# Kernel tuning notes

Hardware: AMD Instinct MI355X
Metric: run time of the kernel (lower is better)

## Reference

```python
import jax, jax.numpy as jnp
import numpy as np

B, N, C, H = 16, 4096, 256, 4
D = C // H


def setup_inputs() -> dict:
    key = jax.random.key(0)
    ks = jax.random.split(key, 16)
    s = 0.02
    inp = {
        "x": jax.random.normal(ks[0], (B, N, C), jnp.float32),
        "encoding": jax.random.normal(ks[1], (2, B, 1, N, D), jnp.float32),
        "Wqkv_w": jax.random.normal(ks[2], (3 * C, C), jnp.float32) * s,
        "Wqkv_b": jnp.zeros((3 * C,), jnp.float32),
        "tssa_qkv_w": jax.random.normal(ks[3], (C, C), jnp.float32) * s,
        "tssa_qkv_b": jnp.zeros((C,), jnp.float32),
        "temp": jnp.ones((H, 1), jnp.float32),
        "tssa_out_w": jax.random.normal(ks[4], (C, C), jnp.float32) * s,
        "tssa_out_b": jnp.zeros((C,), jnp.float32),
        "out_proj_w": jax.random.normal(ks[5], (C, C), jnp.float32) * s,
        "out_proj_b": jnp.zeros((C,), jnp.float32),
        "ffn1_w": jax.random.normal(ks[6], (2 * C, 2 * C), jnp.float32) * s,
        "ffn1_b": jnp.zeros((2 * C,), jnp.float32),
        "ln_g": jnp.ones((2 * C,), jnp.float32),
        "ln_b": jnp.zeros((2 * C,), jnp.float32),
        "ffn2_w": jax.random.normal(ks[7], (C, 2 * C), jnp.float32) * s,
        "ffn2_b": jnp.zeros((C,), jnp.float32),
    }
    return inp


def _rotate_half(t):
    # (..., d) -> pairwise rotate: (x1, x2) -> (-x2, x1)
    t2 = t.reshape(t.shape[:-1] + (-1, 2))
    x1, x2 = t2[..., 0], t2[..., 1]
    return jnp.stack((-x2, x1), axis=-1).reshape(t.shape)


def reference(x, encoding, Wqkv_w, Wqkv_b, tssa_qkv_w, tssa_qkv_b, temp,
              tssa_out_w, tssa_out_b, out_proj_w, out_proj_b,
              ffn1_w, ffn1_b, ln_g, ln_b, ffn2_w, ffn2_b):
    b, n, c = x.shape
    h, d = H, D
    # QKV projection, layout (h, d, 3) on last dim as in unflatten(-1,(h,-1,3))
    qkv = (x @ Wqkv_w.T + Wqkv_b).reshape(b, n, h, d, 3).transpose(0, 2, 1, 3, 4)  # b h n d 3
    q, k, v = qkv[..., 0], qkv[..., 1], qkv[..., 2]
    rope = lambda t: t * encoding[0] + _rotate_half(t) * encoding[1]
    q = rope(q)
    k = rope(k)
    flat = lambda t: t.transpose(0, 2, 1, 3).reshape(b, n, c)  # b h n d -> b n (h d)
    w_input = (flat(q) + flat(k) + flat(v)) / 3.0
    # TSSA attention
    w = (w_input @ tssa_qkv_w.T + tssa_qkv_b).reshape(b, n, h, d).transpose(0, 2, 1, 3)  # b h n d
    norm = jnp.sqrt(jnp.sum(w * w, axis=2, keepdims=True))  # L2 over sequence axis N
    w_normed = w / jnp.maximum(norm, 1e-12)
    sum_ws = jnp.sum(w_normed * w_normed, axis=-1)  # b h n
    Pi = jax.nn.softmax(sum_ws * temp[None, :, :], axis=1)  # softmax over heads
    Pi_norm = Pi / (jnp.sum(Pi, axis=-1, keepdims=True) + 1e-8)
    dots = jnp.einsum('bhn,bhnd->bh', Pi_norm, w * w)  # (b,h,1,d) summed over d
    attn = 1.0 / (1.0 + dots)  # b h
    out = -(w * Pi[..., None]) * attn[:, :, None, None]  # b h n d
    out = out.transpose(0, 2, 1, 3).reshape(b, n, c)
    context = out @ tssa_out_w.T + tssa_out_b
    message = context @ out_proj_w.T + out_proj_b
    # residual FFN
    cat = jnp.concatenate([x, message], axis=-1)  # b n 2c
    h1 = cat @ ffn1_w.T + ffn1_b
    mu = jnp.mean(h1, axis=-1, keepdims=True)
    var = jnp.mean((h1 - mu) ** 2, axis=-1, keepdims=True)
    ln = (h1 - mu) / jnp.sqrt(var + 1e-5) * ln_g + ln_b
    g = jax.nn.gelu(ln, approximate=False)
    return x + (g @ ffn2_w.T + ffn2_b)
```

## Files before the change

### kernel.cpp

```cpp
#include <hip/hip_runtime.h>
#include <math.h>

#define Bc 16
#define Nc 4096

typedef __attribute__((ext_vector_type(8))) short short8;
typedef __attribute__((ext_vector_type(4))) float floatx4;

__device__ __forceinline__ unsigned short f2bf(float f) {
    union { float f; unsigned int u; } v; v.f = f;
    unsigned int u = v.u;
    return (unsigned short)((u + 0x7fffu + ((u >> 16) & 1u)) >> 16);
}
__device__ __forceinline__ float bf2f(unsigned short u) {
    union { unsigned int u; float f; } v; v.u = ((unsigned int)u) << 16;
    return v.f;
}

__device__ __forceinline__ void gll16(const unsigned short* g, unsigned short* l) {
    __builtin_amdgcn_global_load_lds(
        (const __attribute__((address_space(1))) void*)g,
        (__attribute__((address_space(3))) void*)l,
        16, 0, 0);
}

template <int EPI, typename TOUT>
__global__ __launch_bounds__(512) void gemm_bf(
    const unsigned short* __restrict__ A0, int lda0,
    const unsigned short* __restrict__ A1, int lda1, int K0,
    const unsigned short* __restrict__ W,
    const float* __restrict__ bias,
    const unsigned short* __restrict__ resid_bf,
    const float* __restrict__ Pi,
    const float* __restrict__ attnb,
    float* __restrict__ norm2,
    float* __restrict__ rowstats,
    TOUT* __restrict__ C, int N, int K)
{
    __shared__ alignas(16) unsigned short As[128 * 64];
    __shared__ alignas(16) unsigned short Bs[256 * 64];

    const int t = threadIdx.x;
    const int bn = blockIdx.x, bm = blockIdx.y;
    const int lane = t & 63, wave = t >> 6;
    const int wm = wave >> 2, wn = wave & 3;
    const int quad = lane >> 4, l16 = lane & 15;
    const int rt = t >> 3, st = t & 7;

    floatx4 acc[4][4];
    #pragma unroll
    for (int i = 0; i < 4; ++i)
        #pragma unroll
        for (int j = 0; j < 4; ++j)
            acc[i][j] = (floatx4){0.f, 0.f, 0.f, 0.f};

    for (int k0 = 0; k0 < K; k0 += 64) {
        #pragma unroll
        for (int hh = 0; hh < 2; ++hh) {
            const int row = hh * 64 + rt;
            const int col = k0 + (st ^ (row & 7)) * 8;
            unsigned short* ldsa = As + row * 64 + st * 8;
            const size_t grow = (size_t)bm * 128 + row;
            if constexpr (EPI == 2) {
                const int b = (int)(grow >> 12);
                const int hd = col >> 6;
                const float sc = -Pi[grow * 4 + hd] * attnb[b * 4 + hd];
                const short8 a = *(const short8*)(A0 + grow * (size_t)lda0 + col);
                short8 o;
                #pragma unroll
                for (int j = 0; j < 8; ++j) o[j] = (short)f2bf(bf2f((unsigned short)a[j]) * sc);
                *(short8*)ldsa = o;
            } else {
                const unsigned short* src = (col < K0)
                    ? (A0 + grow * (size_t)lda0 + col)
                    : (A1 + grow * (size_t)lda1 + (col - K0));
                gll16(src, ldsa);
            }
        }
        #pragma unroll
        for (int hh = 0; hh < 4; ++hh) {
            const int row = hh * 64 + rt;
            const int col = k0 + (st ^ (row & 7)) * 8;
            gll16(W + ((size_t)bn * 256 + row) * (size_t)K + col, Bs + row * 64 + st * 8);
        }
        __syncthreads();
        #pragma unroll
        for (int kk = 0; kk < 2; ++kk) {
            short8 af[4], wf[4];
            #pragma unroll
            for (int i = 0; i < 4; ++i) {
                const int ra = wm * 64 + i * 16 + l16;
                af[i] = *(const short8*)(As + ra * 64 + ((quad + kk * 4) ^ (ra & 7)) * 8);
                const int rw = wn * 64 + i * 16 + l16;
                wf[i] = *(const short8*)(Bs + rw * 64 + ((quad + kk * 4) ^ (rw & 7)) * 8);
            }
            #pragma unroll
            for (int mi = 0; mi < 4; ++mi)
                #pragma unroll
                for (int ni = 0; ni < 4; ++ni)
                    acc[mi][ni] = __builtin_amdgcn_mfma_f32_16x16x32_bf16(
                        wf[ni], af[mi], acc[mi][ni], 0, 0, 0);
        }
        __syncthreads();
    }

    float rs[4], rq[4];
    if constexpr (EPI == 4) {
        #pragma unroll
        for (int m = 0; m < 4; ++m) { rs[m] = 0.f; rq[m] = 0.f; }
    }

    #pragma unroll
    for (int mi = 0; mi < 4; ++mi) {
        const size_t row = (size_t)bm * 128 + wm * 64 + mi * 16 + l16;
        #pragma unroll
        for (int ni = 0; ni < 4; ++ni) {
            const int cb = bn * 256 + wn * 64 + ni * 16 + quad * 4;
            const float4 b4 = *(const float4*)(bias + cb);
            float v[4] = {acc[mi][ni][0] + b4.x, acc[mi][ni][1] + b4.y,
                          acc[mi][ni][2] + b4.z, acc[mi][ni][3] + b4.w};
            if constexpr (EPI == 3) {
                const ushort4 xr = *(const ushort4*)(resid_bf + row * (size_t)N + cb);
                v[0] += bf2f(xr.x); v[1] += bf2f(xr.y);
                v[2] += bf2f(xr.z); v[3] += bf2f(xr.w);
            }
            if constexpr (EPI == 4) {
                #pragma unroll
                for (int rg = 0; rg < 4; ++rg) { rs[mi] += v[rg]; rq[mi] += v[rg] * v[rg]; }
            }
            if constexpr (EPI == 1) {
                float cs[4];
                #pragma unroll
                for (int rg = 0; rg < 4; ++rg) cs[rg] = v[rg] * v[rg];
                #pragma unroll
                for (int rg = 0; rg < 4; ++rg) {
                    float s = cs[rg];
                    s += __shfl_xor(s, 1, 64);
                    s += __shfl_xor(s, 2, 64);
                    s += __shfl_xor(s, 4, 64);
                    s += __shfl_xor(s, 8, 64);
                    if (l16 == 0) atomicAdd(&norm2[(bm >> 5) * 256 + cb + rg], s);
                }
            }
            if constexpr (__is_same(TOUT, float)) {
                float4 o; o.x = v[0]; o.y = v[1]; o.z = v[2]; o.w = v[3];
                *(float4*)(C + row * (size_t)N + cb) = o;
            } else {
                ushort4 o;
                o.x = f2bf(v[0]); o.y = f2bf(v[1]); o.z = f2bf(v[2]); o.w = f2bf(v[3]);
                *(ushort4*)(C + row * (size_t)N + cb) = o;
            }
        }
    }
    if constexpr (EPI == 4) {
        #pragma unroll
        for (int mi = 0; mi < 4; ++mi) {
            float s = rs[mi], q = rq[mi];
            s += __shfl_xor(s, 16, 64); s += __shfl_xor(s, 32, 64);
            q += __shfl_xor(q, 16, 64); q += __shfl_xor(q, 32, 64);
            if (quad == 0) {
                const size_t row = (size_t)bm * 128 + wm * 64 + mi * 16 + l16;
                atomicAdd(&rowstats[row * 2], s);
                atomicAdd(&rowstats[row * 2 + 1], q);
            }
        }
    }
}

__global__ __launch_bounds__(256) void gemm_rope(
    const unsigned short* __restrict__ A,
    const unsigned short* __restrict__ Wsv,
    const float* __restrict__ bsv,
    const float* __restrict__ enc,
    unsigned short* __restrict__ wi)
{
    __shared__ alignas(16) unsigned short As[128 * 64];
    __shared__ alignas(16) unsigned short Ss[128 * 64];
    __shared__ alignas(16) unsigned short Vs[128 * 64];

    const int t = threadIdx.x;
    const int bn = blockIdx.x, bm = blockIdx.y;
    const int lane = t & 63, wave = t >> 6;
    const int wm = wave >> 1, wn = wave & 1;
    const int quad = lane >> 4, l16 = lane & 15;
    const int rt = t >> 3, st = t & 7;

    floatx4 accs[4][4], accv[4][4];
    #pragma unroll
    for (int i = 0; i < 4; ++i)
        #pragma unroll
        for (int j = 0; j < 4; ++j) {
            accs[i][j] = (floatx4){0.f, 0.f, 0.f, 0.f};
            accv[i][j] = (floatx4){0.f, 0.f, 0.f, 0.f};
        }

    for (int k0 = 0; k0 < 256; k0 += 64) {
        #pragma unroll
        for (int hh = 0; hh < 4; ++hh) {
            const int row = hh * 32 + rt;
            const int col = k0 + (st ^ (row & 7)) * 8;
            gll16(A + ((size_t)bm * 128 + row) * 256 + col, As + row * 64 + st * 8);
            gll16(Wsv + (size_t)(bn * 128 + row) * 256 + col, Ss + row * 64 + st * 8);
            gll16(Wsv + (size_t)(256 + bn * 128 + row) * 256 + col, Vs + row * 64 + st * 8);
        }
        __syncthreads();
        #pragma unroll
        for (int kk = 0; kk < 2; ++kk) {
            short8 af[4], sf[4], vf[4];
            #pragma unroll
            for (int i = 0; i < 4; ++i) {
                const int ra = wm * 64 + i * 16 + l16;
                af[i] = *(const short8*)(As + ra * 64 + ((quad + kk * 4) ^ (ra & 7)) * 8);
                const int rw = wn * 64 + i * 16 + l16;
                sf[i] = *(const short8*)(Ss + rw * 64 + ((quad + kk * 4) ^ (rw & 7)) * 8);
                vf[i] = *(const short8*)(Vs + rw * 64 + ((quad + kk * 4) ^ (rw & 7)) * 8);
            }
            #pragma unroll
            for (int mi = 0; mi < 4; ++mi)
                #pragma unroll
                for (int ni = 0; ni < 4; ++ni) {
                    accs[mi][ni] = __builtin_amdgcn_mfma_f32_16x16x32_bf16(sf[ni], af[mi], accs[mi][ni], 0, 0, 0);
                    accv[mi][ni] = __builtin_amdgcn_mfma_f32_16x16x32_bf16(vf[ni], af[mi], accv[mi][ni], 0, 0, 0);
                }
        }
        __syncthreads();
    }

    #pragma unroll
    for (int mi = 0; mi < 4; ++mi) {
        const size_t row = (size_t)bm * 128 + wm * 64 + mi * 16 + l16;
        #pragma unroll
        for (int ni = 0; ni < 4; ++ni) {
            const int cb = bn * 128 + wn * 64 + ni * 16 + quad * 4;
            const int d = cb & 63;
            const float s0 = accs[mi][ni][0] + bsv[cb];
            const float s1 = accs[mi][ni][1] + bsv[cb + 1];
            const float s2 = accs[mi][ni][2] + bsv[cb + 2];
            const float s3 = accs[mi][ni][3] + bsv[cb + 3];
            const float v0 = accv[mi][ni][0] + bsv[256 + cb];
            const float v1 = accv[mi][ni][1] + bsv[256 + cb + 1];
            const float v2 = accv[mi][ni][2] + bsv[256 + cb + 2];
            const float v3 = accv[mi][ni][3] + bsv[256 + cb + 3];
            const float4 e0q = *(const float4*)(enc + row * 64 + d);
            const float4 e1q = *(const float4*)(enc + 4194304 + row * 64 + d);
            const float r0 = s0 * e0q.x - s1 * e1q.x;
            const float r1 = s1 * e0q.y + s0 * e1q.y;
            const float r2 = s2 * e0q.z - s3 * e1q.z;
            const float r3 = s3 * e0q.w + s2 * e1q.w;
            ushort4 o;
            o.x = f2bf((r0 + v0) * (1.f / 3.f));
            o.y = f2bf((r1 + v1) * (1.f / 3.f));
            o.z = f2bf((r2 + v2) * (1.f / 3.f));
            o.w = f2bf((r3 + v3) * (1.f / 3.f));
            *(ushort4*)(wi + row * 256 + cb) = o;
        }
    }
}

__global__ __launch_bounds__(256) void lngelu_kernel(unsigned short* __restrict__ h1,
                                                     const float* __restrict__ rowstats,
                                                     const float* __restrict__ g,
                                                     const float* __restrict__ bb) {
    const size_t gid = (size_t)blockIdx.x * 256 + threadIdx.x;
    const size_t row = gid >> 6;
    const int col = (int)(gid & 63) * 8;
    const float2 stv = *(const float2*)(rowstats + row * 2);
    const float mean = stv.x * (1.f / 512.f);
    const float var = stv.y * (1.f / 512.f) - mean * mean;
    const float rstd = rsqrtf(var + 1e-5f);
    unsigned short* p = h1 + row * 512 + col;
    const short8 hv = *(const short8*)p;
    const float4 g0 = *(const float4*)(g + col);
    const float4 g1 = *(const float4*)(g + col + 4);
    const float4 b0 = *(const float4*)(bb + col);
    const float4 b1 = *(const float4*)(bb + col + 4);
    const float vg[8] = {g0.x, g0.y, g0.z, g0.w, g1.x, g1.y, g1.z, g1.w};
    const float vb[8] = {b0.x, b0.y, b0.z, b0.w, b1.x, b1.y, b1.z, b1.w};
    short8 ov;
    #pragma unroll
    for (int k = 0; k < 8; ++k) {
        const float ln = (bf2f((unsigned short)hv[k]) - mean) * rstd * vg[k] + vb[k];
        ov[k] = (short)f2bf(0.5f * ln * (1.f + erff(ln * 0.70710678118654752f)));
    }
    *(short8*)p = ov;
}

__device__ __forceinline__ void conv8(const float* src, unsigned short* dst, int i) {
    const float4 f0 = *(const float4*)(src + (size_t)i * 8);
    const float4 f1 = *(const float4*)(src + (size_t)i * 8 + 4);
    short8 sv;
    sv[0] = (short)f2bf(f0.x); sv[1] = (short)f2bf(f0.y);
    sv[2] = (short)f2bf(f0.z); sv[3] = (short)f2bf(f0.w);
    sv[4] = (short)f2bf(f1.x); sv[5] = (short)f2bf(f1.y);
    sv[6] = (short)f2bf(f1.z); sv[7] = (short)f2bf(f1.w);
    *(short8*)(dst + (size_t)i * 8) = sv;
}

__global__ __launch_bounds__(256) void prep_all(
    const float* __restrict__ x, const float* __restrict__ Wqkv,
    const float* __restrict__ bqkv, const float* __restrict__ tssa_w,
    const float* __restrict__ op_w, const float* __restrict__ to_w,
    const float* __restrict__ to_b, const float* __restrict__ op_b,
    const float* __restrict__ f1w, const float* __restrict__ f2w,
    unsigned short* __restrict__ x_bf, unsigned short* __restrict__ Wsv,
    float* __restrict__ bsv, unsigned short* __restrict__ tssa_bf,
    unsigned short* __restrict__ Wf, float* __restrict__ bfb,
    unsigned short* __restrict__ ffn1_bf, unsigned short* __restrict__ ffn2_bf,
    float* __restrict__ zbase, float* __restrict__ rowstats)
{
    const int blk = blockIdx.x, tt = threadIdx.x;
    if (blk < 8192) {
        conv8(x, x_bf, blk * 256 + tt);
    } else if (blk < 8704) {
        const int r = blk - 8192, c = tt;
        const int cd = r & 255;
        const int h = cd >> 6, dd = cd & 63;
        const int base = h * 192 + dd * 3;
        if (r < 256) {
            Wsv[r * 256 + c] = f2bf(Wqkv[(base + 0) * 256 + c] + Wqkv[(base + 1) * 256 + c]);
            if (c == 0) bsv[r] = bqkv[base] + bqkv[base + 1];
        } else {
            Wsv[r * 256 + c] = f2bf(Wqkv[(base + 2) * 256 + c]);
            if (c == 0) bsv[r] = bqkv[base + 2];
        }
    } else if (blk < 8960) {
        const int i = blk - 8704;
        float s = 0.f;
        for (int k = 0; k < 256; ++k) s += op_w[i * 256 + k] * to_w[k * 256 + tt];
        Wf[i * 256 + tt] = f2bf(s);
    } else if (blk == 8960) {
        float s = op_b[tt];
        for (int k = 0; k < 256; ++k) s += op_w[tt * 256 + k] * to_b[k];
        bfb[tt] = s;
    } else if (blk < 8993) {
        conv8(tssa_w, tssa_bf, (blk - 8961) * 256 + tt);
    } else if (blk < 9121) {
        conv8(f1w, ffn1_bf, (blk - 8993) * 256 + tt);
    } else if (blk < 9185) {
        conv8(f2w, ffn2_bf, (blk - 9121) * 256 + tt);
    } else {
        const int i = (blk - 9185) * 256 + tt;
        if (i < 4288) zbase[i] = 0.f;
        else if (i < 135360) rowstats[i - 4288] = 0.f;
    }
}

__global__ __launch_bounds__(256) void pi_kernel(const unsigned short* __restrict__ w,
                                                 const float* __restrict__ norm2,
                                                 const float* __restrict__ temp,
                                                 float* __restrict__ Pi,
                                                 float* __restrict__ S,
                                                 float* __restrict__ T) {
    const int t = threadIdx.x;
    const int i = t & 15;
    const int lr = t >> 4;
    const size_t r = (size_t)blockIdx.x * 16 + lr;
    const int b = (int)(r >> 12);
    const unsigned short* wrow = w + r * 256;
    const float* n2row = norm2 + b * 256;
    float raw[4], nrm[4];
    #pragma unroll
    for (int h = 0; h < 4; ++h) {
        const ushort4 wv = *(const ushort4*)(wrow + h * 64 + i * 4);
        const float w0 = bf2f(wv.x), w1 = bf2f(wv.y), w2 = bf2f(wv.z), w3 = bf2f(wv.w);
        const float4 n2 = *(const float4*)(n2row + h * 64 + i * 4);
        const float s0 = w0 * w0, s1 = w1 * w1, s2 = w2 * w2, s3 = w3 * w3;
        raw[h] = s0 + s1 + s2 + s3;
        nrm[h] = s0 / fmaxf(n2.x, 1e-24f) + s1 / fmaxf(n2.y, 1e-24f)
               + s2 / fmaxf(n2.z, 1e-24f) + s3 / fmaxf(n2.w, 1e-24f);
    }
    #pragma unroll
    for (int off = 1; off < 16; off <<= 1) {
        #pragma unroll
        for (int h = 0; h < 4; ++h) {
            raw[h] += __shfl_xor(raw[h], off, 64);
            nrm[h] += __shfl_xor(nrm[h], off, 64);
        }
    }
    float sw[4], m = -1e30f;
    #pragma unroll
    for (int h = 0; h < 4; ++h) { sw[h] = nrm[h] * temp[h]; m = fmaxf(m, sw[h]); }
    float e[4], Z = 0.f;
    #pragma unroll
    for (int h = 0; h < 4; ++h) { e[h] = expf(sw[h] - m); Z += e[h]; }
    const float invZ = 1.f / Z;
    float pi[4];
    #pragma unroll
    for (int h = 0; h < 4; ++h) pi[h] = e[h] * invZ;
    if (i < 4) Pi[r * 4 + i] = pi[i];

    __shared__ float sS[16][4], sT[16][4];
    if (i == 0) {
        #pragma unroll
        for (int h = 0; h < 4; ++h) { sS[lr][h] = pi[h]; sT[lr][h] = pi[h] * raw[h]; }
    }
    __syncthreads();
    if (t < 4) {
        float as = 0.f, at = 0.f;
        for (int rr = 0; rr < 16; ++rr) { as += sS[rr][t]; at += sT[rr][t]; }
        atomicAdd(&S[b * 4 + t], as);
        atomicAdd(&T[b * 4 + t], at);
    }
}

__global__ void attn_kernel(const float* __restrict__ S, const float* __restrict__ T,
                            float* __restrict__ attn) {
    const int i = threadIdx.x;
    const float dots = T[i] / (S[i] + 1e-8f);
    attn[i] = 1.f / (1.f + dots);
}

extern "C" void kernel_launch(void* const* d_in, const int* in_sizes, int n_in,
                              void* d_out, int out_size, void* d_ws, size_t ws_size,
                              hipStream_t stream) {
    (void)in_sizes; (void)n_in; (void)out_size; (void)ws_size;
    const float* x          = (const float*)d_in[0];
    const float* enc        = (const float*)d_in[1];
    const float* Wqkv_w     = (const float*)d_in[2];
    const float* Wqkv_b     = (const float*)d_in[3];
    const float* tssa_qkv_w = (const float*)d_in[4];
    const float* tssa_qkv_b = (const float*)d_in[5];
    const float* temp       = (const float*)d_in[6];
    const float* tssa_out_w = (const float*)d_in[7];
    const float* tssa_out_b = (const float*)d_in[8];
    const float* out_proj_w = (const float*)d_in[9];
    const float* out_proj_b = (const float*)d_in[10];
    const float* ffn1_w     = (const float*)d_in[11];
    const float* ffn1_b     = (const float*)d_in[12];
    const float* ln_g       = (const float*)d_in[13];
    const float* ln_b       = (const float*)d_in[14];
    const float* ffn2_w     = (const float*)d_in[15];
    const float* ffn2_b     = (const float*)d_in[16];
    float* outp = (float*)d_out;

    const int M = Bc * Nc;

    char* ws = (char*)d_ws;
    unsigned short* x_bf  = (unsigned short*)(ws);
    unsigned short* wi_bf = (unsigned short*)(ws + (size_t)(32 << 20));
    unsigned short* h1_bf = (unsigned short*)(ws + (size_t)(32 << 20));
    unsigned short* w_bf  = (unsigned short*)(ws + (size_t)(64 << 20));
    unsigned short* msg_bf= (unsigned short*)(ws + (size_t)(96 << 20));
    float* fb    = (float*)(ws + (size_t)(128 << 20));
    float* Pi    = fb;
    float* norm2 = Pi + 262144;
    float* Sb    = norm2 + 4096;
    float* Tb    = Sb + 64;
    float* attnb = Tb + 64;
    float* bsv   = attnb + 64;
    float* bfb   = bsv + 512;
    float* rowstats = bfb + 256;
    unsigned short* Wsv_bf  = (unsigned short*)(rowstats + 131072);
    unsigned short* tssa_bf = Wsv_bf + 131072;
    unsigned short* Wf_bf   = tssa_bf + 65536;
    unsigned short* ffn1_bf = Wf_bf + 65536;
    unsigned short* ffn2_bf = ffn1_bf + 262144;

    prep_all<<<9714, 256, 0, stream>>>(
        x, Wqkv_w, Wqkv_b, tssa_qkv_w, out_proj_w, tssa_out_w, tssa_out_b,
        out_proj_b, ffn1_w, ffn2_w,
        x_bf, Wsv_bf, bsv, tssa_bf, Wf_bf, bfb, ffn1_bf, ffn2_bf,
        norm2, rowstats);

    gemm_rope<<<dim3(2, M / 128), 256, 0, stream>>>(x_bf, Wsv_bf, bsv, enc, wi_bf);

    gemm_bf<1, unsigned short><<<dim3(1, M / 128), 512, 0, stream>>>(
        wi_bf, 256, wi_bf, 256, 256, tssa_bf, tssa_qkv_b,
        nullptr, nullptr, nullptr, norm2, nullptr, w_bf, 256, 256);

    pi_kernel<<<4096, 256, 0, stream>>>(w_bf, norm2, temp, Pi, Sb, Tb);
    attn_kernel<<<1, 64, 0, stream>>>(Sb, Tb, attnb);

    gemm_bf<2, unsigned short><<<dim3(1, M / 128), 512, 0, stream>>>(
        w_bf, 256, w_bf, 256, 256, Wf_bf, bfb,
        nullptr, Pi, attnb, nullptr, nullptr, msg_bf, 256, 256);

    gemm_bf<4, unsigned short><<<dim3(2, M / 128), 512, 0, stream>>>(
        x_bf, 256, msg_bf, 256, 256, ffn1_bf, ffn1_b,
        nullptr, nullptr, nullptr, nullptr, rowstats, h1_bf, 512, 512);

    lngelu_kernel<<<16384, 256, 0, stream>>>(h1_bf, rowstats, ln_g, ln_b);

    gemm_bf<3, float><<<dim3(1, M / 128), 512, 0, stream>>>(
        h1_bf, 512, h1_bf, 512, 512, ffn2_bf, ffn2_b,
        x_bf, nullptr, nullptr, nullptr, nullptr, outp, 256, 512);
}
```

Measured before the change: 456.7 us.

## Replace custom rope GEMM with generic gemm_bf epilogue and fold attn into consumer

```diff
diff --git a/kernel.cpp b/kernel.cpp
--- a/kernel.cpp
+++ b/kernel.cpp
@@ -32,7 +32,9 @@
     const float* __restrict__ bias,
     const unsigned short* __restrict__ resid_bf,
     const float* __restrict__ Pi,
-    const float* __restrict__ attnb,
+    const float* __restrict__ Sb,
+    const float* __restrict__ Tb,
+    const float* __restrict__ enc,
     float* __restrict__ norm2,
     float* __restrict__ rowstats,
     TOUT* __restrict__ C, int N, int K)
@@ -64,7 +66,9 @@
             if constexpr (EPI == 2) {
                 const int b = (int)(grow >> 12);
                 const int hd = col >> 6;
-                const float sc = -Pi[grow * 4 + hd] * attnb[b * 4 + hd];
+                const float s = Sb[b * 4 + hd] + 1e-8f;
+                const float at = s / (s + Tb[b * 4 + hd]);
+                const float sc = -Pi[grow * 4 + hd] * at;
                 const short8 a = *(const short8*)(A0 + grow * (size_t)lda0 + col);
                 short8 o;
                 #pragma unroll
@@ -117,6 +121,23 @@
         for (int ni = 0; ni < 4; ++ni) {
             const int cb = bn * 256 + wn * 64 + ni * 16 + quad * 4;
             const float4 b4 = *(const float4*)(bias + cb);
+            if constexpr (EPI == 5) {
+                const int j = cb >> 2;
+                const int h = j >> 5, d = (j & 31) * 2;
+                const float s0 = acc[mi][ni][0] + b4.x;
+                const float s1 = acc[mi][ni][1] + b4.y;
+                const float v0 = acc[mi][ni][2] + b4.z;
+                const float v1 = acc[mi][ni][3] + b4.w;
+                const float2 e0 = *(const float2*)(enc + row * 64 + d);
+                const float2 e1 = *(const float2*)(enc + 4194304 + row * 64 + d);
+                const float r0 = s0 * e0.x - s1 * e1.x;
+                const float r1 = s1 * e0.y + s0 * e1.y;
+                ushort2 o;
+                o.x = f2bf((r0 + v0) * (1.f / 3.f));
+                o.y = f2bf((r1 + v1) * (1.f / 3.f));
+                *(ushort2*)((unsigned short*)C + row * 256 + h * 64 + d) = o;
+                continue;
+            }
             float v[4] = {acc[mi][ni][0] + b4.x, acc[mi][ni][1] + b4.y,
                           acc[mi][ni][2] + b4.z, acc[mi][ni][3] + b4.w};
             if constexpr (EPI == 3) {
@@ -129,12 +150,9 @@
                 for (int rg = 0; rg < 4; ++rg) { rs[mi] += v[rg]; rq[mi] += v[rg] * v[rg]; }
             }
             if constexpr (EPI == 1) {
-                float cs[4];
-                #pragma unroll
-                for (int rg = 0; rg < 4; ++rg) cs[rg] = v[rg] * v[rg];
                 #pragma unroll
                 for (int rg = 0; rg < 4; ++rg) {
-                    float s = cs[rg];
+                    float s = v[rg] * v[rg];
                     s += __shfl_xor(s, 1, 64);
                     s += __shfl_xor(s, 2, 64);
                     s += __shfl_xor(s, 4, 64);
@@ -163,96 +181,6 @@
                 atomicAdd(&rowstats[row * 2], s);
                 atomicAdd(&rowstats[row * 2 + 1], q);
             }
-        }
-    }
-}
-
-__global__ __launch_bounds__(256) void gemm_rope(
-    const unsigned short* __restrict__ A,
-    const unsigned short* __restrict__ Wsv,
-    const float* __restrict__ bsv,
-    const float* __restrict__ enc,
-    unsigned short* __restrict__ wi)
-{
-    __shared__ alignas(16) unsigned short As[128 * 64];
-    __shared__ alignas(16) unsigned short Ss[128 * 64];
-    __shared__ alignas(16) unsigned short Vs[128 * 64];
-
-    const int t = threadIdx.x;
-    const int bn = blockIdx.x, bm = blockIdx.y;
-    const int lane = t & 63, wave = t >> 6;
-    const int wm = wave >> 1, wn = wave & 1;
-    const int quad = lane >> 4, l16 = lane & 15;
-    const int rt = t >> 3, st = t & 7;
-
-    floatx4 accs[4][4], accv[4][4];
-    #pragma unroll
-    for (int i = 0; i < 4; ++i)
-        #pragma unroll
-        for (int j = 0; j < 4; ++j) {
-            accs[i][j] = (floatx4){0.f, 0.f, 0.f, 0.f};
-            accv[i][j] = (floatx4){0.f, 0.f, 0.f, 0.f};
-        }
-
-    for (int k0 = 0; k0 < 256; k0 += 64) {
-        #pragma unroll
-        for (int hh = 0; hh < 4; ++hh) {
-            const int row = hh * 32 + rt;
-            const int col = k0 + (st ^ (row & 7)) * 8;
-            gll16(A + ((size_t)bm * 128 + row) * 256 + col, As + row * 64 + st * 8);
-            gll16(Wsv + (size_t)(bn * 128 + row) * 256 + col, Ss + row * 64 + st * 8);
-            gll16(Wsv + (size_t)(256 + bn * 128 + row) * 256 + col, Vs + row * 64 + st * 8);
-        }
-        __syncthreads();
-        #pragma unroll
-        for (int kk = 0; kk < 2; ++kk) {
-            short8 af[4], sf[4], vf[4];
-            #pragma unroll
-            for (int i = 0; i < 4; ++i) {
-                const int ra = wm * 64 + i * 16 + l16;
-                af[i] = *(const short8*)(As + ra * 64 + ((quad + kk * 4) ^ (ra & 7)) * 8);
-                const int rw = wn * 64 + i * 16 + l16;
-                sf[i] = *(const short8*)(Ss + rw * 64 + ((quad + kk * 4) ^ (rw & 7)) * 8);
-                vf[i] = *(const short8*)(Vs + rw * 64 + ((quad + kk * 4) ^ (rw & 7)) * 8);
-            }
-            #pragma unroll
-            for (int mi = 0; mi < 4; ++mi)
-                #pragma unroll
-                for (int ni = 0; ni < 4; ++ni) {
-                    accs[mi][ni] = __builtin_amdgcn_mfma_f32_16x16x32_bf16(sf[ni], af[mi], accs[mi][ni], 0, 0, 0);
-                    accv[mi][ni] = __builtin_amdgcn_mfma_f32_16x16x32_bf16(vf[ni], af[mi], accv[mi][ni], 0, 0, 0);
-                }
-        }
-        __syncthreads();
-    }
-
-    #pragma unroll
-    for (int mi = 0; mi < 4; ++mi) {
-        const size_t row = (size_t)bm * 128 + wm * 64 + mi * 16 + l16;
-        #pragma unroll
-        for (int ni = 0; ni < 4; ++ni) {
-            const int cb = bn * 128 + wn * 64 + ni * 16 + quad * 4;
-            const int d = cb & 63;
-            const float s0 = accs[mi][ni][0] + bsv[cb];
-            const float s1 = accs[mi][ni][1] + bsv[cb + 1];
-            const float s2 = accs[mi][ni][2] + bsv[cb + 2];
-            const float s3 = accs[mi][ni][3] + bsv[cb + 3];
-            const float v0 = accv[mi][ni][0] + bsv[256 + cb];
-            const float v1 = accv[mi][ni][1] + bsv[256 + cb + 1];
-            const float v2 = accv[mi][ni][2] + bsv[256 + cb + 2];
-            const float v3 = accv[mi][ni][3] + bsv[256 + cb + 3];
-            const float4 e0q = *(const float4*)(enc + row * 64 + d);
-            const float4 e1q = *(const float4*)(enc + 4194304 + row * 64 + d);
-            const float r0 = s0 * e0q.x - s1 * e1q.x;
-            const float r1 = s1 * e0q.y + s0 * e1q.y;
-            const float r2 = s2 * e0q.z - s3 * e1q.z;
-            const float r3 = s3 * e0q.w + s2 * e1q.w;
-            ushort4 o;
-            o.x = f2bf((r0 + v0) * (1.f / 3.f));
-            o.y = f2bf((r1 + v1) * (1.f / 3.f));
-            o.z = f2bf((r2 + v2) * (1.f / 3.f));
-            o.w = f2bf((r3 + v3) * (1.f / 3.f));
-            *(ushort4*)(wi + row * 256 + cb) = o;
         }
     }
 }
@@ -302,8 +230,8 @@
     const float* __restrict__ op_w, const float* __restrict__ to_w,
     const float* __restrict__ to_b, const float* __restrict__ op_b,
     const float* __restrict__ f1w, const float* __restrict__ f2w,
-    unsigned short* __restrict__ x_bf, unsigned short* __restrict__ Wsv,
-    float* __restrict__ bsv, unsigned short* __restrict__ tssa_bf,
+    unsigned short* __restrict__ x_bf, unsigned short* __restrict__ Wsvq,
+    float* __restrict__ bsvq, unsigned short* __restrict__ tssa_bf,
     unsigned short* __restrict__ Wf, float* __restrict__ bfb,
     unsigned short* __restrict__ ffn1_bf, unsigned short* __restrict__ ffn2_bf,
     float* __restrict__ zbase, float* __restrict__ rowstats)
@@ -313,15 +241,16 @@
         conv8(x, x_bf, blk * 256 + tt);
     } else if (blk < 8704) {
         const int r = blk - 8192, c = tt;
-        const int cd = r & 255;
-        const int h = cd >> 6, dd = cd & 63;
+        const int j = r >> 2, m = r & 3;
+        const int cc = 2 * j + (m & 1);
+        const int h = cc >> 6, dd = cc & 63;
         const int base = h * 192 + dd * 3;
-        if (r < 256) {
-            Wsv[r * 256 + c] = f2bf(Wqkv[(base + 0) * 256 + c] + Wqkv[(base + 1) * 256 + c]);
-            if (c == 0) bsv[r] = bqkv[base] + bqkv[base + 1];
+        if (m < 2) {
+            Wsvq[r * 256 + c] = f2bf(Wqkv[(base + 0) * 256 + c] + Wqkv[(base + 1) * 256 + c]);
+            if (c == 0) bsvq[r] = bqkv[base] + bqkv[base + 1];
         } else {
-            Wsv[r * 256 + c] = f2bf(Wqkv[(base + 2) * 256 + c]);
-            if (c == 0) bsv[r] = bqkv[base + 2];
+            Wsvq[r * 256 + c] = f2bf(Wqkv[(base + 2) * 256 + c]);
+            if (c == 0) bsvq[r] = bqkv[base + 2];
         }
     } else if (blk < 8960) {
         const int i = blk - 8704;
@@ -401,13 +330,6 @@
         atomicAdd(&S[b * 4 + t], as);
         atomicAdd(&T[b * 4 + t], at);
     }
-}
-
-__global__ void attn_kernel(const float* __restrict__ S, const float* __restrict__ T,
-                            float* __restrict__ attn) {
-    const int i = threadIdx.x;
-    const float dots = T[i] / (S[i] + 1e-8f);
-    attn[i] = 1.f / (1.f + dots);
 }
 
 extern "C" void kernel_launch(void* const* d_in, const int* in_sizes, int n_in,
@@ -447,11 +369,11 @@
     float* Sb    = norm2 + 4096;
     float* Tb    = Sb + 64;
     float* attnb = Tb + 64;
-    float* bsv   = attnb + 64;
-    float* bfb   = bsv + 512;
+    float* bsvq  = attnb + 64;
+    float* bfb   = bsvq + 512;
     float* rowstats = bfb + 256;
-    unsigned short* Wsv_bf  = (unsigned short*)(rowstats + 131072);
-    unsigned short* tssa_bf = Wsv_bf + 131072;
+    unsigned short* Wsvq_bf = (unsigned short*)(rowstats + 131072);
+    unsigned short* tssa_bf = Wsvq_bf + 131072;
     unsigned short* Wf_bf   = tssa_bf + 65536;
     unsigned short* ffn1_bf = Wf_bf + 65536;
     unsigned short* ffn2_bf = ffn1_bf + 262144;
@@ -459,29 +381,35 @@
     prep_all<<<9714, 256, 0, stream>>>(
         x, Wqkv_w, Wqkv_b, tssa_qkv_w, out_proj_w, tssa_out_w, tssa_out_b,
         out_proj_b, ffn1_w, ffn2_w,
-        x_bf, Wsv_bf, bsv, tssa_bf, Wf_bf, bfb, ffn1_bf, ffn2_bf,
+        x_bf, Wsvq_bf, bsvq, tssa_bf, Wf_bf, bfb, ffn1_bf, ffn2_bf,
         norm2, rowstats);
 
-    gemm_rope<<<dim3(2, M / 128), 256, 0, stream>>>(x_bf, Wsv_bf, bsv, enc, wi_bf);
+    gemm_bf<5, unsigned short><<<dim3(2, M / 128), 512, 0, stream>>>(
+        x_bf, 256, x_bf, 256, 256, Wsvq_bf, bsvq,
+        nullptr, nullptr, nullptr, nullptr, enc, nullptr, nullptr,
+        wi_bf, 256, 256);
 
     gemm_bf<1, unsigned short><<<dim3(1, M / 128), 512, 0, stream>>>(
         wi_bf, 256, wi_bf, 256, 256, tssa_bf, tssa_qkv_b,
-        nullptr, nullptr, nullptr, norm2, nullptr, w_bf, 256, 256);
+        nullptr, nullptr, nullptr, nullptr, nullptr, norm2, nullptr,
+        w_bf, 256, 256);
 
     pi_kernel<<<4096, 256, 0, stream>>>(w_bf, norm2, temp, Pi, Sb, Tb);
-    attn_kernel<<<1, 64, 0, stream>>>(Sb, Tb, attnb);
 
     gemm_bf<2, unsigned short><<<dim3(1, M / 128), 512, 0, stream>>>(
         w_bf, 256, w_bf, 256, 256, Wf_bf, bfb,
-        nullptr, Pi, attnb, nullptr, nullptr, msg_bf, 256, 256);
+        nullptr, Pi, Sb, Tb, nullptr, nullptr, nullptr,
+        msg_bf, 256, 256);
 
     gemm_bf<4, unsigned short><<<dim3(2, M / 128), 512, 0, stream>>>(
         x_bf, 256, msg_bf, 256, 256, ffn1_bf, ffn1_b,
-        nullptr, nullptr, nullptr, nullptr, rowstats, h1_bf, 512, 512);
+        nullptr, nullptr, nullptr, nullptr, nullptr, nullptr, rowstats,
+        h1_bf, 512, 512);
 
     lngelu_kernel<<<16384, 256, 0, stream>>>(h1_bf, rowstats, ln_g, ln_b);
 
     gemm_bf<3, float><<<dim3(1, M / 128), 512, 0, stream>>>(
         h1_bf, 512, h1_bf, 512, 512, ffn2_bf, ffn2_b,
-        x_bf, nullptr, nullptr, nullptr, nullptr, outp, 256, 512);
-}
+        x_bf, nullptr, nullptr, nullptr, nullptr, nullptr, nullptr,
+        outp, 256, 512);
+}
```

Result: slower. 472.8 us (+3.5%).
